# Kernel tuning notes

Measured on AMD Instinct MI355X. Metric: run time of the kernel, lower is better.

## Reference

```python
import jax, jax.numpy as jnp
import numpy as np

B, T, C = 4, 2048, 1024
H = 16
D = C // H  # 64


def setup_inputs() -> dict:
    key = jax.random.key(0)
    ks = jax.random.split(key, 3)
    scale = 1.0 / np.sqrt(C)
    return {
        "x": jax.random.normal(ks[0], (B, T, C), dtype=jnp.float32),
        "W_attn": jax.random.normal(ks[1], (C, 3 * C), dtype=jnp.float32) * scale,
        "b_attn": jnp.zeros((3 * C,), dtype=jnp.float32),
        "W_proj": jax.random.normal(ks[2], (C, C), dtype=jnp.float32) * scale,
        "b_proj": jnp.zeros((C,), dtype=jnp.float32),
    }


def reference(x, W_attn, b_attn, W_proj, b_proj):
    b, t, c = x.shape
    qkv = x @ W_attn + b_attn                      # [B,T,3C]
    q, k, v = jnp.split(qkv, 3, axis=-1)           # each [B,T,C]
    to_heads = lambda z: z.reshape(b, t, H, D).transpose(0, 2, 1, 3)  # [B,H,T,D]
    q, k, v = to_heads(q), to_heads(k), to_heads(v)
    scores = jnp.einsum("bhtd,bhsd->bhts", q, k) / jnp.sqrt(jnp.float32(D))
    causal = jnp.tril(jnp.ones((t, t), dtype=bool))  # [T,T]
    scores = jnp.where(causal[None, None], scores, jnp.finfo(scores.dtype).min)
    attn = jax.nn.softmax(scores, axis=-1)           # [B,H,T,T]
    out = jnp.einsum("bhts,bhsd->bhtd", attn, v)     # [B,H,T,D]
    out = out.transpose(0, 2, 1, 3).reshape(b, t, c)
    return out @ W_proj + b_proj
```

## Files before the change

kernel.cpp:

```cpp
#include <hip/hip_runtime.h>
#include <hip/hip_bf16.h>

typedef __bf16 bf16_t;
typedef __attribute__((ext_vector_type(8))) __bf16 bf16x8;
typedef __attribute__((ext_vector_type(4))) float f32x4;
typedef __attribute__((ext_vector_type(4))) unsigned short u16x4;

#define B_DIM 4
#define T_DIM 2048
#define C_DIM 1024
#define H_DIM 16
#define D_DIM 64
#define M_TOK (B_DIM * T_DIM)
#define N_QKV (3 * C_DIM)
#define NT    (T_DIM / 64)
#define KSTR  72
#define CSC   0.18033688011112042f

__device__ __forceinline__ void gload_lds16(const bf16_t* g, bf16_t* l) {
  __builtin_amdgcn_global_load_lds((const __attribute__((address_space(1))) void*)(g),
                                   (__attribute__((address_space(3))) void*)(l), 16, 0, 0);
}

__global__ void cvt_f32_to_bf16(const float* __restrict__ in, bf16_t* __restrict__ out, int n4) {
  int i = blockIdx.x * blockDim.x + threadIdx.x;
  if (i >= n4) return;
  float4 v = ((const float4*)in)[i];
  struct alignas(8) bv4 { bf16_t x, y, z, w; };
  bv4 o;
  o.x = (bf16_t)v.x; o.y = (bf16_t)v.y; o.z = (bf16_t)v.z; o.w = (bf16_t)v.w;
  ((bv4*)out)[i] = o;
}

__global__ void transpose_f32_to_bf16(const float* __restrict__ in, bf16_t* __restrict__ out,
                                      int K, int N) {
  __shared__ float tile[32][33];
  int bx = blockIdx.x * 32;
  int by = blockIdx.y * 32;
  int tx = threadIdx.x, ty = threadIdx.y;
#pragma unroll
  for (int i = 0; i < 32; i += 8)
    tile[ty + i][tx] = in[(size_t)(by + ty + i) * N + bx + tx];
  __syncthreads();
#pragma unroll
  for (int i = 0; i < 32; i += 8)
    out[(size_t)(bx + ty + i) * K + by + tx] = (bf16_t)tile[tx][ty + i];
}

#define BM 128
#define BN 128
#define BK 32

__global__ __launch_bounds__(256)
void gemm_bt_bias(const bf16_t* __restrict__ A, const bf16_t* __restrict__ Bt,
                  const float* __restrict__ bias, bf16_t* __restrict__ Cb,
                  float* __restrict__ Cf, int M, int N, int K) {
  __shared__ alignas(16) bf16_t As[BM * BK];
  __shared__ alignas(16) bf16_t Bs[BN * BK];
  const int tid = threadIdx.x;
  const int lane = tid & 63;
  const int wave = tid >> 6;
  const int wr = (wave >> 1) * 64, wc = (wave & 1) * 64;
  const int quad = lane >> 4, l16 = lane & 15;
  const int row0 = blockIdx.x * BM, col0 = blockIdx.y * BN;

  const int srow = wave * 32 + (lane >> 2);
  const int scol = (lane & 3) * 8;
  const bf16_t* Ag = A + (size_t)(row0 + srow) * K + scol;
  const bf16_t* Bg = Bt + (size_t)(col0 + srow) * K + scol;
  bf16_t* AsW = &As[(wave * 32) * BK];
  bf16_t* BsW = &Bs[(wave * 32) * BK];

  f32x4 acc[4][4];
#pragma unroll
  for (int i = 0; i < 4; ++i)
#pragma unroll
    for (int j = 0; j < 4; ++j)
      acc[i][j] = (f32x4){0.f, 0.f, 0.f, 0.f};

  for (int k0 = 0; k0 < K; k0 += BK) {
    __syncthreads();
    gload_lds16(Ag + k0, AsW);
    gload_lds16(Ag + k0 + (size_t)16 * K, AsW + 16 * BK);
    gload_lds16(Bg + k0, BsW);
    gload_lds16(Bg + k0 + (size_t)16 * K, BsW + 16 * BK);
    __syncthreads();
    bf16x8 af[4], bfr[4];
#pragma unroll
    for (int i = 0; i < 4; ++i)
      af[i] = *(const bf16x8*)&As[(wr + i * 16 + l16) * BK + quad * 8];
#pragma unroll
    for (int j = 0; j < 4; ++j)
      bfr[j] = *(const bf16x8*)&Bs[(wc + j * 16 + l16) * BK + quad * 8];
#pragma unroll
    for (int i = 0; i < 4; ++i)
#pragma unroll
      for (int j = 0; j < 4; ++j)
        acc[i][j] = __builtin_amdgcn_mfma_f32_16x16x32_bf16(af[i], bfr[j], acc[i][j], 0, 0, 0);
  }

#pragma unroll
  for (int i = 0; i < 4; ++i)
#pragma unroll
    for (int j = 0; j < 4; ++j) {
      int col = col0 + wc + j * 16 + l16;
      float bv = bias[col];
#pragma unroll
      for (int r = 0; r < 4; ++r) {
        int row = row0 + wr + i * 16 + quad * 4 + r;
        float v = acc[i][j][r] + bv;
        if (Cb) Cb[(size_t)row * N + col] = (bf16_t)v;
        else    Cf[(size_t)row * N + col] = v;
      }
    }
}

__device__ __forceinline__ void softmax_step(f32x4 sv[4], float& m_st, float& l_st,
                                             f32x4 o_acc[4], bool diag, bf16_t* PsW,
                                             int l16, int quad, int wave) {
  if (diag) {
    const int qr = wave * 16 + l16;
#pragma unroll
    for (int ct = 0; ct < 4; ++ct)
#pragma unroll
      for (int r = 0; r < 4; ++r)
        if (ct * 16 + quad * 4 + r > qr) sv[ct][r] = -INFINITY;
  }
  float rmax = sv[0][0];
#pragma unroll
  for (int ct = 0; ct < 4; ++ct)
#pragma unroll
    for (int r = 0; r < 4; ++r) rmax = fmaxf(rmax, sv[ct][r]);
  rmax = fmaxf(rmax, __shfl_xor(rmax, 16));
  rmax = fmaxf(rmax, __shfl_xor(rmax, 32));
  float m_new = fmaxf(m_st, rmax);
  float alpha = __builtin_amdgcn_exp2f((m_st - m_new) * CSC);
  float mc = m_new * CSC;
  float rsum = 0.f;
#pragma unroll
  for (int ct = 0; ct < 4; ++ct) {
    u16x4 pk;
#pragma unroll
    for (int r = 0; r < 4; ++r) {
      float p = __builtin_amdgcn_exp2f(__builtin_fmaf(sv[ct][r], CSC, -mc));
      rsum += p;
      pk[r] = __builtin_bit_cast(unsigned short, (bf16_t)p);
    }
    *(u16x4*)&PsW[l16 * KSTR + ct * 16 + quad * 4] = pk;
  }
  rsum += __shfl_xor(rsum, 16);
  rsum += __shfl_xor(rsum, 32);
  l_st = l_st * alpha + rsum;
  m_st = m_new;
#pragma unroll
  for (int dt = 0; dt < 4; ++dt)
#pragma unroll
    for (int r = 0; r < 4; ++r) o_acc[dt][r] *= alpha;
}

__global__ __launch_bounds__(256, 4)
void attn_fwd(const bf16_t* __restrict__ qkv, bf16_t* __restrict__ out) {
  __shared__ alignas(16) bf16_t Ks[64 * KSTR];
  __shared__ alignas(16) bf16_t Vt[64 * KSTR];
  __shared__ alignas(16) bf16_t Ps[4 * 16 * KSTR];

  const int tid = threadIdx.x;
  const int lane = tid & 63;
  const int wave = tid >> 6;
  const int quad = lane >> 4, l16 = lane & 15;
  const int qlo = blockIdx.x;
  const int qhi = NT - 1 - qlo;
  const int h = blockIdx.y, b = blockIdx.z;
  const size_t tokBase = (size_t)b * T_DIM;

  const bf16_t* qpl = qkv + (tokBase + qlo * 64 + wave * 16 + l16) * N_QKV + h * D_DIM;
  const bf16_t* qph = qkv + (tokBase + qhi * 64 + wave * 16 + l16) * N_QKV + h * D_DIM;
  bf16x8 ql0 = *(const bf16x8*)(qpl + quad * 8);
  bf16x8 ql1 = *(const bf16x8*)(qpl + 32 + quad * 8);
  bf16x8 qh0 = *(const bf16x8*)(qph + quad * 8);
  bf16x8 qh1 = *(const bf16x8*)(qph + 32 + quad * 8);

  f32x4 ol[4], oh[4];
#pragma unroll
  for (int dt = 0; dt < 4; ++dt) {
    ol[dt] = (f32x4){0.f, 0.f, 0.f, 0.f};
    oh[dt] = (f32x4){0.f, 0.f, 0.f, 0.f};
  }
  float ml = -INFINITY, ll = 0.f, mh = -INFINITY, lh = 0.f;

  const int tx = tid & 15, ty = tid >> 4;
  bf16_t* PsW = &Ps[wave * 16 * KSTR];
  const f32x4 zero4 = (f32x4){0.f, 0.f, 0.f, 0.f};

  u16x4 kreg[4], vreg[4];
  const bf16_t* kb0 = qkv + (tokBase + ty * 4) * N_QKV + h * D_DIM + C_DIM + tx * 4;
#pragma unroll
  for (int r = 0; r < 4; ++r) kreg[r] = *(const u16x4*)(kb0 + (size_t)r * N_QKV);
#pragma unroll
  for (int r = 0; r < 4; ++r) vreg[r] = *(const u16x4*)(kb0 + (size_t)r * N_QKV + C_DIM);

  for (int t = 0; t <= qhi; ++t) {
    const bool lo = (t <= qlo);
    __syncthreads();
#pragma unroll
    for (int r = 0; r < 4; ++r)
      *(u16x4*)&Ks[(ty * 4 + r) * KSTR + tx * 4] = kreg[r];
#pragma unroll
    for (int i = 0; i < 4; ++i) {
      u16x4 p = (u16x4){vreg[0][i], vreg[1][i], vreg[2][i], vreg[3][i]};
      *(u16x4*)&Vt[(tx * 4 + i) * KSTR + ty * 4] = p;
    }
    __syncthreads();
    if (t < qhi) {
      const bf16_t* kb = qkv + (tokBase + (t + 1) * 64 + ty * 4) * N_QKV + h * D_DIM + C_DIM + tx * 4;
#pragma unroll
      for (int r = 0; r < 4; ++r) kreg[r] = *(const u16x4*)(kb + (size_t)r * N_QKV);
#pragma unroll
      for (int r = 0; r < 4; ++r) vreg[r] = *(const u16x4*)(kb + (size_t)r * N_QKV + C_DIM);
    }

    f32x4 svl[4], svh[4];
#pragma unroll
    for (int ct = 0; ct < 4; ++ct) {
      bf16x8 kf0 = *(const bf16x8*)&Ks[(ct * 16 + l16) * KSTR + quad * 8];
      bf16x8 kf1 = *(const bf16x8*)&Ks[(ct * 16 + l16) * KSTR + 32 + quad * 8];
      if (lo) {
        svl[ct] = __builtin_amdgcn_mfma_f32_16x16x32_bf16(kf0, ql0, zero4, 0, 0, 0);
        svl[ct] = __builtin_amdgcn_mfma_f32_16x16x32_bf16(kf1, ql1, svl[ct], 0, 0, 0);
      }
      svh[ct] = __builtin_amdgcn_mfma_f32_16x16x32_bf16(kf0, qh0, zero4, 0, 0, 0);
      svh[ct] = __builtin_amdgcn_mfma_f32_16x16x32_bf16(kf1, qh1, svh[ct], 0, 0, 0);
    }

    bf16x8 pl0, pl1, ph0, ph1;
    if (lo) {
      softmax_step(svl, ml, ll, ol, t == qlo, PsW, l16, quad, wave);
      pl0 = *(const bf16x8*)&PsW[l16 * KSTR + quad * 8];
      pl1 = *(const bf16x8*)&PsW[l16 * KSTR + 32 + quad * 8];
    }
    softmax_step(svh, mh, lh, oh, t == qhi, PsW, l16, quad, wave);
    ph0 = *(const bf16x8*)&PsW[l16 * KSTR + quad * 8];
    ph1 = *(const bf16x8*)&PsW[l16 * KSTR + 32 + quad * 8];

#pragma unroll
    for (int dt = 0; dt < 4; ++dt) {
      bf16x8 vf0 = *(const bf16x8*)&Vt[(dt * 16 + l16) * KSTR + quad * 8];
      bf16x8 vf1 = *(const bf16x8*)&Vt[(dt * 16 + l16) * KSTR + 32 + quad * 8];
      if (lo) {
        ol[dt] = __builtin_amdgcn_mfma_f32_16x16x32_bf16(vf0, pl0, ol[dt], 0, 0, 0);
        ol[dt] = __builtin_amdgcn_mfma_f32_16x16x32_bf16(vf1, pl1, ol[dt], 0, 0, 0);
      }
      oh[dt] = __builtin_amdgcn_mfma_f32_16x16x32_bf16(vf0, ph0, oh[dt], 0, 0, 0);
      oh[dt] = __builtin_amdgcn_mfma_f32_16x16x32_bf16(vf1, ph1, oh[dt], 0, 0, 0);
    }
  }

  struct alignas(8) bh4 { bf16_t a, b, c, d; };
  {
    float rl = 1.0f / ll;
    bf16_t* op = out + (tokBase + qlo * 64 + wave * 16 + l16) * C_DIM + h * D_DIM;
#pragma unroll
    for (int dt = 0; dt < 4; ++dt) {
      bh4 v = {(bf16_t)(ol[dt][0] * rl), (bf16_t)(ol[dt][1] * rl),
               (bf16_t)(ol[dt][2] * rl), (bf16_t)(ol[dt][3] * rl)};
      *(bh4*)(op + dt * 16 + quad * 4) = v;
    }
  }
  {
    float rl = 1.0f / lh;
    bf16_t* op = out + (tokBase + qhi * 64 + wave * 16 + l16) * C_DIM + h * D_DIM;
#pragma unroll
    for (int dt = 0; dt < 4; ++dt) {
      bh4 v = {(bf16_t)(oh[dt][0] * rl), (bf16_t)(oh[dt][1] * rl),
               (bf16_t)(oh[dt][2] * rl), (bf16_t)(oh[dt][3] * rl)};
      *(bh4*)(op + dt * 16 + quad * 4) = v;
    }
  }
}

extern "C" void kernel_launch(void* const* d_in, const int* in_sizes, int n_in,
                              void* d_out, int out_size, void* d_ws, size_t ws_size,
                              hipStream_t stream) {
  const float* x      = (const float*)d_in[0];
  const float* W_attn = (const float*)d_in[1];
  const float* b_attn = (const float*)d_in[2];
  const float* W_proj = (const float*)d_in[3];
  const float* b_proj = (const float*)d_in[4];
  float* out = (float*)d_out;

  char* ws = (char*)d_ws;
  bf16_t* xb   = (bf16_t*)ws;  ws += (size_t)M_TOK * C_DIM * 2;
  bf16_t* Wat  = (bf16_t*)ws;  ws += (size_t)N_QKV * C_DIM * 2;
  bf16_t* Wpt  = (bf16_t*)ws;  ws += (size_t)C_DIM * C_DIM * 2;
  bf16_t* qkv  = (bf16_t*)ws;  ws += (size_t)M_TOK * N_QKV * 2;
  bf16_t* attn = (bf16_t*)ws;  ws += (size_t)M_TOK * C_DIM * 2;

  {
    int n4 = (M_TOK * C_DIM) / 4;
    cvt_f32_to_bf16<<<n4 / 256, 256, 0, stream>>>(x, xb, n4);
  }
  transpose_f32_to_bf16<<<dim3(N_QKV / 32, C_DIM / 32), dim3(32, 8), 0, stream>>>(W_attn, Wat, C_DIM, N_QKV);
  transpose_f32_to_bf16<<<dim3(C_DIM / 32, C_DIM / 32), dim3(32, 8), 0, stream>>>(W_proj, Wpt, C_DIM, C_DIM);

  gemm_bt_bias<<<dim3(M_TOK / BM, N_QKV / BN), 256, 0, stream>>>(
      xb, Wat, b_attn, qkv, nullptr, M_TOK, N_QKV, C_DIM);

  attn_fwd<<<dim3(NT / 2, H_DIM, B_DIM), 256, 0, stream>>>(qkv, attn);

  gemm_bt_bias<<<dim3(M_TOK / BM, C_DIM / BN), 256, 0, stream>>>(
      attn, Wpt, b_proj, nullptr, out, M_TOK, C_DIM, C_DIM);
}
```

Before: 295.6 us.

## Add 128x64 projection GEMM, split softmax P buffers, pack bf16 stores

Adds a dedicated output-projection GEMM with 128x64 tiles, doubling the block count for the N=1024 projection so the GPU is better filled. The attention kernel gets separate LDS P buffers for the low and high query tiles, letting both softmax steps run before the P reads. LDS use goes up in exchange. bf16 packing now goes through 32-bit pairs for stores in several kernels, and the QKV GEMM gains a launch-bounds occupancy hint with its branchy epilogue removed.

After: 289.5 us. 1.02x faster.

```diff
diff --git a/kernel.cpp b/kernel.cpp
--- a/kernel.cpp
+++ b/kernel.cpp
@@ -5,6 +5,7 @@
 typedef __attribute__((ext_vector_type(8))) __bf16 bf16x8;
 typedef __attribute__((ext_vector_type(4))) float f32x4;
 typedef __attribute__((ext_vector_type(4))) unsigned short u16x4;
+typedef __attribute__((ext_vector_type(2))) unsigned int u32x2;
 
 #define B_DIM 4
 #define T_DIM 2048
@@ -22,14 +23,17 @@
                                    (__attribute__((address_space(3))) void*)(l), 16, 0, 0);
 }
 
+__device__ __forceinline__ unsigned int pk_bf16(float a, float b) {
+  unsigned short lo = __builtin_bit_cast(unsigned short, (bf16_t)a);
+  unsigned short hi = __builtin_bit_cast(unsigned short, (bf16_t)b);
+  return (unsigned int)lo | ((unsigned int)hi << 16);
+}
+
 __global__ void cvt_f32_to_bf16(const float* __restrict__ in, bf16_t* __restrict__ out, int n4) {
   int i = blockIdx.x * blockDim.x + threadIdx.x;
   if (i >= n4) return;
   float4 v = ((const float4*)in)[i];
-  struct alignas(8) bv4 { bf16_t x, y, z, w; };
-  bv4 o;
-  o.x = (bf16_t)v.x; o.y = (bf16_t)v.y; o.z = (bf16_t)v.z; o.w = (bf16_t)v.w;
-  ((bv4*)out)[i] = o;
+  ((u32x2*)out)[i] = (u32x2){pk_bf16(v.x, v.y), pk_bf16(v.z, v.w)};
 }
 
 __global__ void transpose_f32_to_bf16(const float* __restrict__ in, bf16_t* __restrict__ out,
@@ -51,10 +55,10 @@
 #define BN 128
 #define BK 32
 
-__global__ __launch_bounds__(256)
+__global__ __launch_bounds__(256, 4)
 void gemm_bt_bias(const bf16_t* __restrict__ A, const bf16_t* __restrict__ Bt,
                   const float* __restrict__ bias, bf16_t* __restrict__ Cb,
-                  float* __restrict__ Cf, int M, int N, int K) {
+                  int M, int N, int K) {
   __shared__ alignas(16) bf16_t As[BM * BK];
   __shared__ alignas(16) bf16_t Bs[BN * BK];
   const int tid = threadIdx.x;
@@ -108,9 +112,68 @@
 #pragma unroll
       for (int r = 0; r < 4; ++r) {
         int row = row0 + wr + i * 16 + quad * 4 + r;
-        float v = acc[i][j][r] + bv;
-        if (Cb) Cb[(size_t)row * N + col] = (bf16_t)v;
-        else    Cf[(size_t)row * N + col] = v;
+        Cb[(size_t)row * N + col] = (bf16_t)(acc[i][j][r] + bv);
+      }
+    }
+}
+
+__global__ __launch_bounds__(256, 4)
+void gemm_bt_bias_n64(const bf16_t* __restrict__ A, const bf16_t* __restrict__ Bt,
+                      const float* __restrict__ bias, float* __restrict__ Cf,
+                      int M, int N, int K) {
+  __shared__ alignas(16) bf16_t As[BM * BK];
+  __shared__ alignas(16) bf16_t Bs[64 * BK];
+  const int tid = threadIdx.x;
+  const int lane = tid & 63;
+  const int wave = tid >> 6;
+  const int wr = (wave >> 1) * 64, wc = (wave & 1) * 32;
+  const int quad = lane >> 4, l16 = lane & 15;
+  const int row0 = blockIdx.x * BM, col0 = blockIdx.y * 64;
+
+  const int sr = lane >> 2;
+  const int scol = (lane & 3) * 8;
+  const bf16_t* Ag = A + (size_t)(row0 + wave * 32 + sr) * K + scol;
+  const bf16_t* Bg = Bt + (size_t)(col0 + wave * 16 + sr) * K + scol;
+  bf16_t* AsW = &As[(wave * 32) * BK];
+  bf16_t* BsW = &Bs[(wave * 16) * BK];
+
+  f32x4 acc[4][2];
+#pragma unroll
+  for (int i = 0; i < 4; ++i)
+#pragma unroll
+    for (int j = 0; j < 2; ++j)
+      acc[i][j] = (f32x4){0.f, 0.f, 0.f, 0.f};
+
+  for (int k0 = 0; k0 < K; k0 += BK) {
+    __syncthreads();
+    gload_lds16(Ag + k0, AsW);
+    gload_lds16(Ag + k0 + (size_t)16 * K, AsW + 16 * BK);
+    gload_lds16(Bg + k0, BsW);
+    __syncthreads();
+    bf16x8 af[4], bfr[2];
+#pragma unroll
+    for (int i = 0; i < 4; ++i)
+      af[i] = *(const bf16x8*)&As[(wr + i * 16 + l16) * BK + quad * 8];
+#pragma unroll
+    for (int j = 0; j < 2; ++j)
+      bfr[j] = *(const bf16x8*)&Bs[(wc + j * 16 + l16) * BK + quad * 8];
+#pragma unroll
+    for (int i = 0; i < 4; ++i)
+#pragma unroll
+      for (int j = 0; j < 2; ++j)
+        acc[i][j] = __builtin_amdgcn_mfma_f32_16x16x32_bf16(af[i], bfr[j], acc[i][j], 0, 0, 0);
+  }
+
+#pragma unroll
+  for (int i = 0; i < 4; ++i)
+#pragma unroll
+    for (int j = 0; j < 2; ++j) {
+      int col = col0 + wc + j * 16 + l16;
+      float bv = bias[col];
+#pragma unroll
+      for (int r = 0; r < 4; ++r) {
+        int row = row0 + wr + i * 16 + quad * 4 + r;
+        Cf[(size_t)row * N + col] = acc[i][j][r] + bv;
       }
     }
 }
@@ -139,14 +202,14 @@
   float rsum = 0.f;
 #pragma unroll
   for (int ct = 0; ct < 4; ++ct) {
-    u16x4 pk;
+    float p[4];
 #pragma unroll
     for (int r = 0; r < 4; ++r) {
-      float p = __builtin_amdgcn_exp2f(__builtin_fmaf(sv[ct][r], CSC, -mc));
-      rsum += p;
-      pk[r] = __builtin_bit_cast(unsigned short, (bf16_t)p);
-    }
-    *(u16x4*)&PsW[l16 * KSTR + ct * 16 + quad * 4] = pk;
+      p[r] = __builtin_amdgcn_exp2f(__builtin_fmaf(sv[ct][r], CSC, -mc));
+      rsum += p[r];
+    }
+    u32x2 pk = (u32x2){pk_bf16(p[0], p[1]), pk_bf16(p[2], p[3])};
+    *(u32x2*)&PsW[l16 * KSTR + ct * 16 + quad * 4] = pk;
   }
   rsum += __shfl_xor(rsum, 16);
   rsum += __shfl_xor(rsum, 32);
@@ -162,7 +225,7 @@
 void attn_fwd(const bf16_t* __restrict__ qkv, bf16_t* __restrict__ out) {
   __shared__ alignas(16) bf16_t Ks[64 * KSTR];
   __shared__ alignas(16) bf16_t Vt[64 * KSTR];
-  __shared__ alignas(16) bf16_t Ps[4 * 16 * KSTR];
+  __shared__ alignas(16) bf16_t Ps[4 * 2 * 16 * KSTR];
 
   const int tid = threadIdx.x;
   const int lane = tid & 63;
@@ -189,7 +252,8 @@
   float ml = -INFINITY, ll = 0.f, mh = -INFINITY, lh = 0.f;
 
   const int tx = tid & 15, ty = tid >> 4;
-  bf16_t* PsW = &Ps[wave * 16 * KSTR];
+  bf16_t* PsL = &Ps[(wave * 2 + 0) * 16 * KSTR];
+  bf16_t* PsH = &Ps[(wave * 2 + 1) * 16 * KSTR];
   const f32x4 zero4 = (f32x4){0.f, 0.f, 0.f, 0.f};
 
   u16x4 kreg[4], vreg[4];
@@ -232,15 +296,16 @@
       svh[ct] = __builtin_amdgcn_mfma_f32_16x16x32_bf16(kf1, qh1, svh[ct], 0, 0, 0);
     }
 
+    if (lo) softmax_step(svl, ml, ll, ol, t == qlo, PsL, l16, quad, wave);
+    softmax_step(svh, mh, lh, oh, t == qhi, PsH, l16, quad, wave);
+
     bf16x8 pl0, pl1, ph0, ph1;
     if (lo) {
-      softmax_step(svl, ml, ll, ol, t == qlo, PsW, l16, quad, wave);
-      pl0 = *(const bf16x8*)&PsW[l16 * KSTR + quad * 8];
-      pl1 = *(const bf16x8*)&PsW[l16 * KSTR + 32 + quad * 8];
-    }
-    softmax_step(svh, mh, lh, oh, t == qhi, PsW, l16, quad, wave);
-    ph0 = *(const bf16x8*)&PsW[l16 * KSTR + quad * 8];
-    ph1 = *(const bf16x8*)&PsW[l16 * KSTR + 32 + quad * 8];
+      pl0 = *(const bf16x8*)&PsL[l16 * KSTR + quad * 8];
+      pl1 = *(const bf16x8*)&PsL[l16 * KSTR + 32 + quad * 8];
+    }
+    ph0 = *(const bf16x8*)&PsH[l16 * KSTR + quad * 8];
+    ph1 = *(const bf16x8*)&PsH[l16 * KSTR + 32 + quad * 8];
 
 #pragma unroll
     for (int dt = 0; dt < 4; ++dt) {
@@ -255,15 +320,14 @@
     }
   }
 
-  struct alignas(8) bh4 { bf16_t a, b, c, d; };
   {
     float rl = 1.0f / ll;
     bf16_t* op = out + (tokBase + qlo * 64 + wave * 16 + l16) * C_DIM + h * D_DIM;
 #pragma unroll
     for (int dt = 0; dt < 4; ++dt) {
-      bh4 v = {(bf16_t)(ol[dt][0] * rl), (bf16_t)(ol[dt][1] * rl),
-               (bf16_t)(ol[dt][2] * rl), (bf16_t)(ol[dt][3] * rl)};
-      *(bh4*)(op + dt * 16 + quad * 4) = v;
+      u32x2 v = (u32x2){pk_bf16(ol[dt][0] * rl, ol[dt][1] * rl),
+                        pk_bf16(ol[dt][2] * rl, ol[dt][3] * rl)};
+      *(u32x2*)(op + dt * 16 + quad * 4) = v;
     }
   }
   {
@@ -271,9 +335,9 @@
     bf16_t* op = out + (tokBase + qhi * 64 + wave * 16 + l16) * C_DIM + h * D_DIM;
 #pragma unroll
     for (int dt = 0; dt < 4; ++dt) {
-      bh4 v = {(bf16_t)(oh[dt][0] * rl), (bf16_t)(oh[dt][1] * rl),
-               (bf16_t)(oh[dt][2] * rl), (bf16_t)(oh[dt][3] * rl)};
-      *(bh4*)(op + dt * 16 + quad * 4) = v;
+      u32x2 v = (u32x2){pk_bf16(oh[dt][0] * rl, oh[dt][1] * rl),
+                        pk_bf16(oh[dt][2] * rl, oh[dt][3] * rl)};
+      *(u32x2*)(op + dt * 16 + quad * 4) = v;
     }
   }
 }
@@ -303,10 +367,10 @@
   transpose_f32_to_bf16<<<dim3(C_DIM / 32, C_DIM / 32), dim3(32, 8), 0, stream>>>(W_proj, Wpt, C_DIM, C_DIM);
 
   gemm_bt_bias<<<dim3(M_TOK / BM, N_QKV / BN), 256, 0, stream>>>(
-      xb, Wat, b_attn, qkv, nullptr, M_TOK, N_QKV, C_DIM);
+      xb, Wat, b_attn, qkv, M_TOK, N_QKV, C_DIM);
 
   attn_fwd<<<dim3(NT / 2, H_DIM, B_DIM), 256, 0, stream>>>(qkv, attn);
 
-  gemm_bt_bias<<<dim3(M_TOK / BM, C_DIM / BN), 256, 0, stream>>>(
-      attn, Wpt, b_proj, nullptr, out, M_TOK, C_DIM, C_DIM);
-}
+  gemm_bt_bias_n64<<<dim3(M_TOK / BM, C_DIM / 64), 256, 0, stream>>>(
+      attn, Wpt, b_proj, out, M_TOK, C_DIM, C_DIM);
+}
```
